# Performance work log

Hardware: AMD Instinct MI355X
Metric: run time of the kernel (lower is better)

## Reference

```python
import jax, jax.numpy as jnp
import numpy as np

N_GAUSS, H, W, SH_DEG = 1024, 256, 256, 3

SH_C0 = 0.28209479177387814
SH_C1 = 0.4886025119029199
SH_C2 = (1.0925484305920792, -1.0925484305920792, 0.31539156525252005,
         -1.0925484305920792, 0.5462742152960396)
SH_C3 = (-0.5900435899266435, 2.890611442640554, -0.4570457994644658,
         0.3731763325901154, -0.4570457994644658, 1.445305721320277,
         -0.5900435899266435)


def eval_sh(shs, dirs):
    # shs: [N,16,3], dirs: [N,3] normalized. Matches computeColorFromSH (deg 3).
    x, y, z = dirs[:, 0:1], dirs[:, 1:2], dirs[:, 2:3]
    res = SH_C0 * shs[:, 0]
    res = res - SH_C1 * y * shs[:, 1] + SH_C1 * z * shs[:, 2] - SH_C1 * x * shs[:, 3]
    xx, yy, zz = x * x, y * y, z * z
    xy, yz, xz = x * y, y * z, x * z
    res = (res + SH_C2[0] * xy * shs[:, 4] + SH_C2[1] * yz * shs[:, 5]
           + SH_C2[2] * (2.0 * zz - xx - yy) * shs[:, 6]
           + SH_C2[3] * xz * shs[:, 7] + SH_C2[4] * (xx - yy) * shs[:, 8])
    res = (res + SH_C3[0] * y * (3.0 * xx - yy) * shs[:, 9]
           + SH_C3[1] * xy * z * shs[:, 10]
           + SH_C3[2] * y * (4.0 * zz - xx - yy) * shs[:, 11]
           + SH_C3[3] * z * (2.0 * zz - 3.0 * xx - 3.0 * yy) * shs[:, 12]
           + SH_C3[4] * x * (4.0 * zz - xx - yy) * shs[:, 13]
           + SH_C3[5] * z * (xx - yy) * shs[:, 14]
           + SH_C3[6] * x * (xx - yy - zz) * shs[:, 15])
    return jnp.maximum(res + 0.5, 0.0)


def render(background, means3D, opacities, scales, rotations, shs,
           view_mat, proj_mat, cam_pos, tan_fovx, tan_fovy, height, width):
    N = means3D.shape[0]
    tanx, tany = tan_fovx[0], tan_fovy[0]
    fx = width / (2.0 * tanx)
    fy = height / (2.0 * tany)

    # --- 3D covariance: Sigma = R diag(s^2) R^T (computeCov3D) ---
    q = rotations / jnp.linalg.norm(rotations, axis=-1, keepdims=True)
    r, x, y, z = q[:, 0], q[:, 1], q[:, 2], q[:, 3]
    R = jnp.stack([
        jnp.stack([1 - 2 * (y * y + z * z), 2 * (x * y - r * z), 2 * (x * z + r * y)], -1),
        jnp.stack([2 * (x * y + r * z), 1 - 2 * (x * x + z * z), 2 * (y * z - r * x)], -1),
        jnp.stack([2 * (x * z - r * y), 2 * (y * z + r * x), 1 - 2 * (x * x + y * y)], -1),
    ], -2)  # [N,3,3]
    M = R * scales[:, None, :]
    Sigma = jnp.einsum('nij,nkj->nik', M, M)  # [N,3,3]

    # --- view transform + EWA 2D covariance (computeCov2D) ---
    t = means3D @ view_mat[:3, :3].T + view_mat[:3, 3]  # [N,3] camera space
    tz = t[:, 2]
    valid_z = tz > 0.2
    tzs = jnp.where(valid_z, tz, 1.0)
    limx, limy = 1.3 * tanx, 1.3 * tany
    tx = jnp.clip(t[:, 0] / tzs, -limx, limx) * tzs
    ty = jnp.clip(t[:, 1] / tzs, -limy, limy) * tzs
    zeros = jnp.zeros_like(tzs)
    J = jnp.stack([
        jnp.stack([fx / tzs, zeros, -fx * tx / (tzs * tzs)], -1),
        jnp.stack([zeros, fy / tzs, -fy * ty / (tzs * tzs)], -1),
    ], -2)  # [N,2,3]
    T2 = jnp.einsum('nij,jk->nik', J, view_mat[:3, :3])
    cov2d = jnp.einsum('nij,njk,nlk->nil', T2, Sigma, T2)  # [N,2,2]
    a = cov2d[:, 0, 0] + 0.3
    c = cov2d[:, 1, 1] + 0.3
    b = cov2d[:, 0, 1]
    det = a * c - b * b
    valid = valid_z & (det > 0)
    inv_det = jnp.where(det > 0, 1.0 / jnp.where(det > 0, det, 1.0), 0.0)
    conic = jnp.stack([c, -b, a], -1) * inv_det[:, None]  # [N,3]

    # --- projection to pixel coords (ndc2Pix) ---
    ph = jnp.concatenate([means3D, jnp.ones((N, 1), means3D.dtype)], -1) @ proj_mat.T
    p_w = 1.0 / (ph[:, 3] + 1e-7)
    px = ((ph[:, 0] * p_w + 1.0) * width - 1.0) * 0.5
    py = ((ph[:, 1] * p_w + 1.0) * height - 1.0) * 0.5

    # --- SH -> RGB ---
    dirs = means3D - cam_pos[None, :]
    dirs = dirs / jnp.linalg.norm(dirs, axis=-1, keepdims=True)
    colors = eval_sh(shs, dirs)  # [N,3]

    # --- global depth sort (front to back) ---
    depth = jnp.where(valid, tz, 1e10)
    order = jnp.argsort(depth)
    px_s, py_s = px[order], py[order]
    conic_s = conic[order]
    opac_s = opacities[order, 0]
    colors_s = colors[order]
    valid_s = valid[order]

    # --- per-pixel alpha and front-to-back compositing (renderCUDA) ---
    ys, xs = jnp.meshgrid(jnp.arange(height, dtype=jnp.float32),
                          jnp.arange(width, dtype=jnp.float32), indexing='ij')
    pixx, pixy = xs.reshape(-1), ys.reshape(-1)  # [P]
    dx = px_s[:, None] - pixx[None, :]  # [N,P]
    dy = py_s[:, None] - pixy[None, :]
    power = (-0.5 * (conic_s[:, 0:1] * dx * dx + conic_s[:, 2:3] * dy * dy)
             - conic_s[:, 1:2] * dx * dy)
    alpha = jnp.minimum(opac_s[:, None] * jnp.exp(jnp.minimum(power, 0.0)), 0.99)
    keep = (power <= 0.0) & (alpha >= 1.0 / 255.0) & valid_s[:, None]
    alpha = jnp.where(keep, alpha, 0.0)

    Tcum = jnp.cumprod(1.0 - alpha, axis=0)  # [N,P]
    T_prev = jnp.concatenate([jnp.ones((1, alpha.shape[1]), alpha.dtype), Tcum[:-1]], 0)
    wgt = alpha * T_prev
    img = jnp.einsum('nc,np->cp', colors_s, wgt) + background[:, None] * Tcum[-1][None, :]
    return img.reshape(3, height, width)


def setup_inputs() -> dict:
    key = jax.random.key(0)
    ks = jax.random.split(key, 6)
    means3D = jax.random.uniform(ks[0], (N_GAUSS, 3), minval=-3.0, maxval=3.0)
    means3D = means3D.at[:, 2].set(
        jax.random.uniform(ks[1], (N_GAUSS,), minval=2.0, maxval=10.0))
    opacities = jax.random.uniform(ks[2], (N_GAUSS, 1), minval=0.3, maxval=0.95)
    scales = jax.random.uniform(ks[3], (N_GAUSS, 3), minval=0.02, maxval=0.15)
    rotations = jax.random.normal(ks[4], (N_GAUSS, 4))
    shs = jax.random.normal(ks[5], (N_GAUSS, (SH_DEG + 1) ** 2, 3)) * 0.3
    background = jnp.zeros((3,), jnp.float32)
    view_mat = jnp.eye(4, dtype=jnp.float32)  # camera at origin looking +z
    tanx = tany = 0.5
    zn, zf = 0.01, 100.0
    proj = np.zeros((4, 4), np.float32)
    proj[0, 0] = 1.0 / tanx
    proj[1, 1] = 1.0 / tany
    proj[2, 2] = zf / (zf - zn)
    proj[2, 3] = -(zf * zn) / (zf - zn)
    proj[3, 2] = 1.0
    proj_mat = jnp.asarray(proj) @ view_mat  # full projection
    cam_pos = jnp.zeros((3,), jnp.float32)
    return dict(background=background, means3D=means3D, opacities=opacities,
                scales=scales, rotations=rotations, shs=shs, view_mat=view_mat,
                proj_mat=proj_mat, cam_pos=cam_pos,
                tan_fovx=jnp.array([tanx], jnp.float32),
                tan_fovy=jnp.array([tany], jnp.float32), height=H, width=W)


def reference(background, means3D, opacities, scales, rotations, shs,
              view_mat, proj_mat, cam_pos, tan_fovx, tan_fovy, height, width):
    return render(background, means3D, opacities, scales, rotations, shs,
                  view_mat, proj_mat, cam_pos, tan_fovx, tan_fovy, height, width)
```

## Files before the change

kernel.cpp:

```cpp
#include <hip/hip_runtime.h>
#include <math.h>

#define NG 1024
#define LOG2E 1.4426950408889634f


__global__ void prep_kernel(
    const float* __restrict__ means3D, const float* __restrict__ opacities,
    const float* __restrict__ scales,  const float* __restrict__ rotations,
    const float* __restrict__ shs,     const float* __restrict__ view_mat,
    const float* __restrict__ proj_mat,const float* __restrict__ cam_pos,
    const float* __restrict__ tanx_p,  const float* __restrict__ tany_p,
    const int* __restrict__ h_p,       const int* __restrict__ w_p,
    unsigned long long* __restrict__ grec, float4* __restrict__ rec, int N)
{
    int i = blockIdx.x * blockDim.x + threadIdx.x;
    if (i >= N) return;
    float tanx = tanx_p[0], tany = tany_p[0];
    float Wf = (float)w_p[0], Hf = (float)h_p[0];
    int tilesX = w_p[0] >> 3, tilesY = h_p[0] >> 3;
    float fx = Wf / (2.f * tanx), fy = Hf / (2.f * tany);

    float mx = means3D[3*i], my = means3D[3*i+1], mz = means3D[3*i+2];

    float4 q4 = ((const float4*)rotations)[i];
    float qr = q4.x, qx = q4.y, qy = q4.z, qz = q4.w;
    float qn = sqrtf(qr*qr + qx*qx + qy*qy + qz*qz);
    qr /= qn; qx /= qn; qy /= qn; qz /= qn;
    float sx = scales[3*i], sy = scales[3*i+1], sz = scales[3*i+2];
    float R00 = 1.f-2.f*(qy*qy+qz*qz), R01 = 2.f*(qx*qy-qr*qz), R02 = 2.f*(qx*qz+qr*qy);
    float R10 = 2.f*(qx*qy+qr*qz), R11 = 1.f-2.f*(qx*qx+qz*qz), R12 = 2.f*(qy*qz-qr*qx);
    float R20 = 2.f*(qx*qz-qr*qy), R21 = 2.f*(qy*qz+qr*qx), R22 = 1.f-2.f*(qx*qx+qy*qy);
    float M00=R00*sx, M01=R01*sy, M02=R02*sz;
    float M10=R10*sx, M11=R11*sy, M12=R12*sz;
    float M20=R20*sx, M21=R21*sy, M22=R22*sz;
    float S00 = M00*M00+M01*M01+M02*M02;
    float S01 = M00*M10+M01*M11+M02*M12;
    float S02 = M00*M20+M01*M21+M02*M22;
    float S11 = M10*M10+M11*M11+M12*M12;
    float S12 = M10*M20+M11*M21+M12*M22;
    float S22 = M20*M20+M21*M21+M22*M22;

    const float* V = view_mat;
    float t0 = V[0]*mx + V[1]*my + V[2]*mz  + V[3];
    float t1 = V[4]*mx + V[5]*my + V[6]*mz  + V[7];
    float t2 = V[8]*mx + V[9]*my + V[10]*mz + V[11];
    bool valid_z = t2 > 0.2f;
    float tzs = valid_z ? t2 : 1.0f;
    float limx = 1.3f*tanx, limy = 1.3f*tany;
    float txc = fminf(fmaxf(t0/tzs, -limx), limx) * tzs;
    float tyc = fminf(fmaxf(t1/tzs, -limy), limy) * tzs;
    float inv_tz = 1.f / tzs;
    float J00 = fx*inv_tz, J02 = -fx*txc*inv_tz*inv_tz;
    float J11 = fy*inv_tz, J12 = -fy*tyc*inv_tz*inv_tz;
    float T200 = J00*V[0] + J02*V[8];
    float T201 = J00*V[1] + J02*V[9];
    float T202 = J00*V[2] + J02*V[10];
    float T210 = J11*V[4] + J12*V[8];
    float T211 = J11*V[5] + J12*V[9];
    float T212 = J11*V[6] + J12*V[10];
    float u0 = S00*T200 + S01*T201 + S02*T202;
    float u1 = S01*T200 + S11*T201 + S12*T202;
    float u2 = S02*T200 + S12*T201 + S22*T202;
    float cov00 = T200*u0 + T201*u1 + T202*u2;
    float cov01 = T210*u0 + T211*u1 + T212*u2;
    float v0 = S00*T210 + S01*T211 + S02*T212;
    float v1 = S01*T210 + S11*T211 + S12*T212;
    float v2 = S02*T210 + S12*T211 + S22*T212;
    float cov11 = T210*v0 + T211*v1 + T212*v2;
    float a = cov00 + 0.3f;
    float c = cov11 + 0.3f;
    float b = cov01;
    float det = a*c - b*b;
    bool valid = valid_z && (det > 0.f);
    float inv_det = (det > 0.f) ? (1.f/det) : 0.f;
    float Aq = c*inv_det, Bq = -b*inv_det, Cq = a*inv_det;

    const float* P = proj_mat;
    float ph0 = P[0]*mx  + P[1]*my  + P[2]*mz  + P[3];
    float ph1 = P[4]*mx  + P[5]*my  + P[6]*mz  + P[7];
    float ph3 = P[12]*mx + P[13]*my + P[14]*mz + P[15];
    float pw = 1.f / (ph3 + 1e-7f);
    float px = ((ph0*pw + 1.f)*Wf - 1.f)*0.5f;
    float py = ((ph1*pw + 1.f)*Hf - 1.f)*0.5f;

    float dxm = mx - cam_pos[0], dym = my - cam_pos[1], dzm = mz - cam_pos[2];
    float dn = sqrtf(dxm*dxm + dym*dym + dzm*dzm);
    float X = dxm/dn, Y = dym/dn, Z = dzm/dn;
    float xx = X*X, yy = Y*Y, zz = Z*Z;
    float xy = X*Y, yz = Y*Z, xz = X*Z;
    float sc[48];
    {
        const float4* s4 = (const float4*)(shs + i*48);
        #pragma unroll
        for (int k = 0; k < 12; k++) {
            float4 v = s4[k];
            sc[4*k] = v.x; sc[4*k+1] = v.y; sc[4*k+2] = v.z; sc[4*k+3] = v.w;
        }
    }
    float col[3];
    #pragma unroll
    for (int ch = 0; ch < 3; ch++) {
        float res = 0.28209479177387814f * sc[ch];
        res += -0.4886025119029199f * Y * sc[3+ch]
             +  0.4886025119029199f * Z * sc[6+ch]
             -  0.4886025119029199f * X * sc[9+ch];
        res +=  1.0925484305920792f * xy * sc[12+ch]
             + (-1.0925484305920792f) * yz * sc[15+ch]
             +  0.31539156525252005f * (2.f*zz - xx - yy) * sc[18+ch]
             + (-1.0925484305920792f) * xz * sc[21+ch]
             +  0.5462742152960396f * (xx - yy) * sc[24+ch];
        res += -0.5900435899266435f * Y * (3.f*xx - yy) * sc[27+ch]
             +  2.890611442640554f  * xy * Z * sc[30+ch]
             + (-0.4570457994644658f) * Y * (4.f*zz - xx - yy) * sc[33+ch]
             +  0.3731763325901154f  * Z * (2.f*zz - 3.f*xx - 3.f*yy) * sc[36+ch]
             + (-0.4570457994644658f) * X * (4.f*zz - xx - yy) * sc[39+ch]
             +  1.445305721320277f   * Z * (xx - yy) * sc[42+ch]
             + (-0.5900435899266435f) * X * (xx - yy - zz) * sc[45+ch];
        col[ch] = fmaxf(res + 0.5f, 0.f);
    }

    float op = valid ? opacities[i] : 0.f;
    float dpt = valid ? t2 : 1e10f;

    float tau = 2.f * logf(255.f * fmaxf(op, 1e-20f));
    bool has = valid && (op * 255.f > 1.f) && (tau > 0.f);
    float rx = has ? (sqrtf(tau * a) + 0.01f) : 0.f;
    float ry = has ? (sqrtf(tau * c) + 0.01f) : 0.f;

    unsigned trange = 31u;
    if (has) {
        int tx0 = (int)ceilf((px - rx - 7.f) * 0.125f);
        int tx1 = (int)floorf((px + rx) * 0.125f);
        int ty0 = (int)ceilf((py - ry - 7.f) * 0.125f);
        int ty1 = (int)floorf((py + ry) * 0.125f);
        tx0 = max(tx0, 0); ty0 = max(ty0, 0);
        tx1 = min(tx1, tilesX - 1); ty1 = min(ty1, tilesY - 1);
        if (tx0 <= tx1 && ty0 <= ty1)
            trange = (unsigned)tx0 | ((unsigned)tx1 << 5)
                   | ((unsigned)ty0 << 10) | ((unsigned)ty1 << 15);
    }
    grec[i] = ((unsigned long long)__float_as_uint(dpt) << 32)
            | ((unsigned long long)(unsigned)i << 20) | trange;

    rec[i*3 + 0] = make_float4(px, py, -0.5f*LOG2E*Aq, -LOG2E*Bq);
    rec[i*3 + 1] = make_float4(-0.5f*LOG2E*Cq, op, col[0], col[1]);
    rec[i*3 + 2] = make_float4(col[2], 0.f, 0.f, 0.f);
}

__device__ inline unsigned long long bstage_shfl(unsigned long long key,
                                                 int tid, int j, int k) {
    unsigned long long partner = __shfl_xor(key, j, 64);
    bool lower = (tid & j) == 0;
    bool asc   = (tid & k) == 0;
    return ((key < partner) == (lower == asc)) ? key : partner;
}

__device__ inline float rlane(float v, int l) {
    return __int_as_float(__builtin_amdgcn_readlane(__float_as_int(v), l));
}

__global__ void __launch_bounds__(64) render_kernel(
    const unsigned long long* __restrict__ grec,
    const float4* __restrict__ rec,
    const float* __restrict__ background,
    float* __restrict__ out,
    int N, int W, int HW)
{
    __shared__ unsigned long long skey[NG];
    int tile = blockIdx.x;
    int tilesX = W >> 3;
    int tx = tile % tilesX, ty = tile / tilesX;
    int lane = threadIdx.x;
    int lx = lane & 7, ly = lane >> 3;
    float pixx = (float)(tx*8 + lx);
    float pixy = (float)(ty*8 + ly);

    int cnt = 0;
    const unsigned long long missk = 31ull;
    for (int base = 0; base < N; base += 256) {
        int g0 = base + lane;
        unsigned long long ka = (g0       < N) ? grec[g0]       : missk;
        unsigned long long kb = (g0 + 64  < N) ? grec[g0 + 64]  : missk;
        unsigned long long kc = (g0 + 128 < N) ? grec[g0 + 128] : missk;
        unsigned long long kd = (g0 + 192 < N) ? grec[g0 + 192] : missk;
        #pragma unroll
        for (int s = 0; s < 4; s++) {
            unsigned long long k = (s == 0) ? ka : (s == 1) ? kb : (s == 2) ? kc : kd;
            unsigned tr = (unsigned)k;
            bool hit = (tx >= (int)(tr & 31u)) & (tx <= (int)((tr >> 5) & 31u))
                     & (ty >= (int)((tr >> 10) & 31u)) & (ty <= (int)((tr >> 15) & 31u));
            unsigned long long mask = __ballot(hit);
            if (hit) {
                int pos = cnt + __popcll(mask & ((1ull << lane) - 1ull));
                skey[pos] = k;
            }
            cnt += __popcll(mask);
        }
    }
    __syncthreads();

    float T = 1.f, Cr = 0.f, Cg = 0.f, Cb = 0.f;
    if (cnt > 0 && cnt <= 64) {
        unsigned long long key = (lane < cnt) ? skey[lane] : ~0ull;
        for (int k = 2; k <= 64; k <<= 1)
            for (int j = k >> 1; j >= 1; j >>= 1)
                key = bstage_shfl(key, lane, j, k);
        int gg = (int)((key >> 20) & (NG - 1));
        float4 r0 = rec[gg*3 + 0];
        float4 r1 = rec[gg*3 + 1];
        float4 r2 = rec[gg*3 + 2];
        for (int m = 0; m < cnt; m++) {
            float gpx = rlane(r0.x, m), gpy = rlane(r0.y, m);
            float gA  = rlane(r0.z, m), gB  = rlane(r0.w, m);
            float gC  = rlane(r1.x, m), gop = rlane(r1.y, m);
            float gcr = rlane(r1.z, m), gcg = rlane(r1.w, m);
            float gcb = rlane(r2.x, m);
            float dx = gpx - pixx, dy = gpy - pixy;
            float p2 = fmaf(gA, dx*dx, fmaf(gC, dy*dy, gB*(dx*dy)));
            float e  = __builtin_amdgcn_exp2f(p2);
            float alpha = fminf(gop * e, 0.99f);
            float a2 = (alpha >= (1.f/255.f)) ? alpha : 0.f;
            float w = a2 * T;
            Cr = fmaf(gcr, w, Cr);
            Cg = fmaf(gcg, w, Cg);
            Cb = fmaf(gcb, w, Cb);
            T  = T - a2 * T;
            if ((m & 15) == 15 && __all(T < 1e-4f)) break;
        }
    } else if (cnt > 64) {
        int P = 128;
        while (P < cnt) P <<= 1;
        for (int i2 = cnt + lane; i2 < P; i2 += 64) skey[i2] = ~0ull;
        __syncthreads();
        for (int k = 2; k <= P; k <<= 1) {
            for (int j = k >> 1; j >= 1; j >>= 1) {
                for (int i2 = lane; i2 < P; i2 += 64) {
                    int ixj = i2 ^ j;
                    if (ixj > i2) {
                        bool asc = (i2 & k) == 0;
                        unsigned long long u = skey[i2], v = skey[ixj];
                        if ((u > v) == asc) { skey[i2] = v; skey[ixj] = u; }
                    }
                }
                __syncthreads();
            }
        }
        bool dead = false;
        for (int c = 0; c < cnt && !dead; c += 64) {
            int len = min(64, cnt - c);
            int idx = c + lane;
            int gg = 0;
            if (idx < cnt) gg = (int)((skey[idx] >> 20) & (NG - 1));
            float4 r0 = rec[gg*3 + 0];
            float4 r1 = rec[gg*3 + 1];
            float4 r2 = rec[gg*3 + 2];
            for (int m = 0; m < len; m++) {
                float gpx = rlane(r0.x, m), gpy = rlane(r0.y, m);
                float gA  = rlane(r0.z, m), gB  = rlane(r0.w, m);
                float gC  = rlane(r1.x, m), gop = rlane(r1.y, m);
                float gcr = rlane(r1.z, m), gcg = rlane(r1.w, m);
                float gcb = rlane(r2.x, m);
                float dx = gpx - pixx, dy = gpy - pixy;
                float p2 = fmaf(gA, dx*dx, fmaf(gC, dy*dy, gB*(dx*dy)));
                float e  = __builtin_amdgcn_exp2f(p2);
                float alpha = fminf(gop * e, 0.99f);
                float a2 = (alpha >= (1.f/255.f)) ? alpha : 0.f;
                float w = a2 * T;
                Cr = fmaf(gcr, w, Cr);
                Cg = fmaf(gcg, w, Cg);
                Cb = fmaf(gcb, w, Cb);
                T  = T - a2 * T;
                if ((m & 15) == 15 && __all(T < 1e-4f)) { dead = true; break; }
            }
            if (__all(T < 1e-4f)) dead = true;
        }
    }

    int p = (ty*8 + ly) * W + tx*8 + lx;
    out[p]        = Cr + background[0]*T;
    out[HW + p]   = Cg + background[1]*T;
    out[2*HW + p] = Cb + background[2]*T;
}

extern "C" void kernel_launch(void* const* d_in, const int* in_sizes, int n_in,
                              void* d_out, int out_size, void* d_ws, size_t ws_size,
                              hipStream_t stream) {
    const float* background = (const float*)d_in[0];
    const float* means3D    = (const float*)d_in[1];
    const float* opacities  = (const float*)d_in[2];
    const float* scales     = (const float*)d_in[3];
    const float* rotations  = (const float*)d_in[4];
    const float* shs        = (const float*)d_in[5];
    const float* view_mat   = (const float*)d_in[6];
    const float* proj_mat   = (const float*)d_in[7];
    const float* cam_pos    = (const float*)d_in[8];
    const float* tanx       = (const float*)d_in[9];
    const float* tany       = (const float*)d_in[10];
    const int*   hp         = (const int*)d_in[11];
    const int*   wp         = (const int*)d_in[12];

    int N  = in_sizes[2];
    int HW = out_size / 3;
    int W  = 256;
    int H  = HW / W;
    float* out = (float*)d_out;

    unsigned long long* grec = (unsigned long long*)d_ws;
    float4* rec = (float4*)(grec + NG);

    prep_kernel<<<16, 64, 0, stream>>>(
        means3D, opacities, scales, rotations, shs, view_mat, proj_mat,
        cam_pos, tanx, tany, hp, wp, grec, rec, N);

    int tiles = (W >> 3) * (H >> 3);
    render_kernel<<<tiles, 64, 0, stream>>>(
        grec, rec, background, out, N, W, HW);
}
```

Baseline: 18.35 us.

## Fuse preprocessing into render kernel, recomputing Gaussian geometry per tile

Removes the separate prep kernel and its global record buffers. Each 8x8 tile block recomputes projection and conic geometry for all 1024 Gaussians to cull them against its own bounds, then recomputes full attributes, including SH color, only for the Gaussians that hit. This trades one kernel launch and a global round trip for heavily redundant per-tile arithmetic (1024 tiles times 1024 Gaussians). The cull now tests a float bounding box rather than integer tile ranges, which can change borderline tile membership.

```diff
diff --git a/kernel.cpp b/kernel.cpp
--- a/kernel.cpp
+++ b/kernel.cpp
@@ -5,22 +5,30 @@
 #define LOG2E 1.4426950408889634f
 
 
-__global__ void prep_kernel(
+__device__ inline unsigned long long bstage_shfl(unsigned long long key,
+                                                 int tid, int j, int k) {
+    unsigned long long partner = __shfl_xor(key, j, 64);
+    bool lower = (tid & j) == 0;
+    bool asc   = (tid & k) == 0;
+    return ((key < partner) == (lower == asc)) ? key : partner;
+}
+
+__device__ inline float rlane(float v, int l) {
+    return __int_as_float(__builtin_amdgcn_readlane(__float_as_int(v), l));
+}
+
+struct Geo {
+    float px, py, rx, ry, dpt, a, b, c, op;
+    bool has;
+};
+
+__device__ inline Geo compute_geo(
+    int i,
     const float* __restrict__ means3D, const float* __restrict__ opacities,
     const float* __restrict__ scales,  const float* __restrict__ rotations,
-    const float* __restrict__ shs,     const float* __restrict__ view_mat,
-    const float* __restrict__ proj_mat,const float* __restrict__ cam_pos,
-    const float* __restrict__ tanx_p,  const float* __restrict__ tany_p,
-    const int* __restrict__ h_p,       const int* __restrict__ w_p,
-    unsigned long long* __restrict__ grec, float4* __restrict__ rec, int N)
+    const float* __restrict__ V,       const float* __restrict__ P,
+    float tanx, float tany, float fx, float fy, float Wf, float Hf)
 {
-    int i = blockIdx.x * blockDim.x + threadIdx.x;
-    if (i >= N) return;
-    float tanx = tanx_p[0], tany = tany_p[0];
-    float Wf = (float)w_p[0], Hf = (float)h_p[0];
-    int tilesX = w_p[0] >> 3, tilesY = h_p[0] >> 3;
-    float fx = Wf / (2.f * tanx), fy = Hf / (2.f * tany);
-
     float mx = means3D[3*i], my = means3D[3*i+1], mz = means3D[3*i+2];
 
     float4 q4 = ((const float4*)rotations)[i];
@@ -41,7 +49,6 @@
     float S12 = M10*M20+M11*M21+M12*M22;
     float S22 = M20*M20+M21*M21+M22*M22;
 
-    const float* V = view_mat;
     float t0 = V[0]*mx + V[1]*my + V[2]*mz  + V[3];
     float t1 = V[4]*mx + V[5]*my + V[6]*mz  + V[7];
     float t2 = V[8]*mx + V[9]*my + V[10]*mz + V[11];
@@ -68,22 +75,51 @@
     float v1 = S01*T210 + S11*T211 + S12*T212;
     float v2 = S02*T210 + S12*T211 + S22*T212;
     float cov11 = T210*v0 + T211*v1 + T212*v2;
-    float a = cov00 + 0.3f;
-    float c = cov11 + 0.3f;
-    float b = cov01;
-    float det = a*c - b*b;
+
+    Geo g;
+    g.a = cov00 + 0.3f;
+    g.c = cov11 + 0.3f;
+    g.b = cov01;
+    float det = g.a*g.c - g.b*g.b;
     bool valid = valid_z && (det > 0.f);
-    float inv_det = (det > 0.f) ? (1.f/det) : 0.f;
-    float Aq = c*inv_det, Bq = -b*inv_det, Cq = a*inv_det;
-
-    const float* P = proj_mat;
+
     float ph0 = P[0]*mx  + P[1]*my  + P[2]*mz  + P[3];
     float ph1 = P[4]*mx  + P[5]*my  + P[6]*mz  + P[7];
     float ph3 = P[12]*mx + P[13]*my + P[14]*mz + P[15];
     float pw = 1.f / (ph3 + 1e-7f);
-    float px = ((ph0*pw + 1.f)*Wf - 1.f)*0.5f;
-    float py = ((ph1*pw + 1.f)*Hf - 1.f)*0.5f;
-
+    g.px = ((ph0*pw + 1.f)*Wf - 1.f)*0.5f;
+    g.py = ((ph1*pw + 1.f)*Hf - 1.f)*0.5f;
+
+    g.op  = valid ? opacities[i] : 0.f;
+    g.dpt = valid ? t2 : 1e10f;
+
+    float tau = 2.f * logf(255.f * fmaxf(g.op, 1e-20f));
+    bool has = valid && (g.op * 255.f > 1.f) && (tau > 0.f);
+    g.rx = has ? (sqrtf(tau * g.a) + 0.01f) : 0.f;
+    g.ry = has ? (sqrtf(tau * g.c) + 0.01f) : 0.f;
+    g.has = has;
+    return g;
+}
+
+__device__ inline void compute_full(
+    int i,
+    const float* __restrict__ means3D, const float* __restrict__ opacities,
+    const float* __restrict__ scales,  const float* __restrict__ rotations,
+    const float* __restrict__ shs,     const float* __restrict__ cam_pos,
+    const float* __restrict__ V,       const float* __restrict__ P,
+    float tanx, float tany, float fx, float fy, float Wf, float Hf,
+    float& px, float& py, float& A2, float& B2, float& C2,
+    float& op, float& cr, float& cg, float& cb)
+{
+    Geo g = compute_geo(i, means3D, opacities, scales, rotations, V, P,
+                        tanx, tany, fx, fy, Wf, Hf);
+    float det = g.a*g.c - g.b*g.b;
+    float inv_det = (det > 0.f) ? (1.f/det) : 0.f;
+    float Aq = g.c*inv_det, Bq = -g.b*inv_det, Cq = g.a*inv_det;
+    px = g.px; py = g.py; op = g.op;
+    A2 = -0.5f*LOG2E*Aq; B2 = -LOG2E*Bq; C2 = -0.5f*LOG2E*Cq;
+
+    float mx = means3D[3*i], my = means3D[3*i+1], mz = means3D[3*i+2];
     float dxm = mx - cam_pos[0], dym = my - cam_pos[1], dzm = mz - cam_pos[2];
     float dn = sqrtf(dxm*dxm + dym*dym + dzm*dzm);
     float X = dxm/dn, Y = dym/dn, Z = dzm/dn;
@@ -119,52 +155,17 @@
              + (-0.5900435899266435f) * X * (xx - yy - zz) * sc[45+ch];
         col[ch] = fmaxf(res + 0.5f, 0.f);
     }
-
-    float op = valid ? opacities[i] : 0.f;
-    float dpt = valid ? t2 : 1e10f;
-
-    float tau = 2.f * logf(255.f * fmaxf(op, 1e-20f));
-    bool has = valid && (op * 255.f > 1.f) && (tau > 0.f);
-    float rx = has ? (sqrtf(tau * a) + 0.01f) : 0.f;
-    float ry = has ? (sqrtf(tau * c) + 0.01f) : 0.f;
-
-    unsigned trange = 31u;
-    if (has) {
-        int tx0 = (int)ceilf((px - rx - 7.f) * 0.125f);
-        int tx1 = (int)floorf((px + rx) * 0.125f);
-        int ty0 = (int)ceilf((py - ry - 7.f) * 0.125f);
-        int ty1 = (int)floorf((py + ry) * 0.125f);
-        tx0 = max(tx0, 0); ty0 = max(ty0, 0);
-        tx1 = min(tx1, tilesX - 1); ty1 = min(ty1, tilesY - 1);
-        if (tx0 <= tx1 && ty0 <= ty1)
-            trange = (unsigned)tx0 | ((unsigned)tx1 << 5)
-                   | ((unsigned)ty0 << 10) | ((unsigned)ty1 << 15);
-    }
-    grec[i] = ((unsigned long long)__float_as_uint(dpt) << 32)
-            | ((unsigned long long)(unsigned)i << 20) | trange;
-
-    rec[i*3 + 0] = make_float4(px, py, -0.5f*LOG2E*Aq, -LOG2E*Bq);
-    rec[i*3 + 1] = make_float4(-0.5f*LOG2E*Cq, op, col[0], col[1]);
-    rec[i*3 + 2] = make_float4(col[2], 0.f, 0.f, 0.f);
-}
-
-__device__ inline unsigned long long bstage_shfl(unsigned long long key,
-                                                 int tid, int j, int k) {
-    unsigned long long partner = __shfl_xor(key, j, 64);
-    bool lower = (tid & j) == 0;
-    bool asc   = (tid & k) == 0;
-    return ((key < partner) == (lower == asc)) ? key : partner;
-}
-
-__device__ inline float rlane(float v, int l) {
-    return __int_as_float(__builtin_amdgcn_readlane(__float_as_int(v), l));
-}
-
-__global__ void __launch_bounds__(64) render_kernel(
-    const unsigned long long* __restrict__ grec,
-    const float4* __restrict__ rec,
-    const float* __restrict__ background,
-    float* __restrict__ out,
+    cr = col[0]; cg = col[1]; cb = col[2];
+}
+
+__global__ void __launch_bounds__(64) fused_kernel(
+    const float* __restrict__ means3D, const float* __restrict__ opacities,
+    const float* __restrict__ scales,  const float* __restrict__ rotations,
+    const float* __restrict__ shs,     const float* __restrict__ view_mat,
+    const float* __restrict__ proj_mat,const float* __restrict__ cam_pos,
+    const float* __restrict__ tanx_p,  const float* __restrict__ tany_p,
+    const int* __restrict__ h_p,       const int* __restrict__ w_p,
+    const float* __restrict__ background, float* __restrict__ out,
     int N, int W, int HW)
 {
     __shared__ unsigned long long skey[NG];
@@ -175,28 +176,34 @@
     int lx = lane & 7, ly = lane >> 3;
     float pixx = (float)(tx*8 + lx);
     float pixy = (float)(ty*8 + ly);
+    float x0 = (float)(tx*8), x1 = x0 + 7.f;
+    float y0 = (float)(ty*8), y1 = y0 + 7.f;
+
+    float tanx = tanx_p[0], tany = tany_p[0];
+    float Wf = (float)w_p[0], Hf = (float)h_p[0];
+    float fx = Wf / (2.f * tanx), fy = Hf / (2.f * tany);
+    const float* V = view_mat;
+    const float* P = proj_mat;
 
     int cnt = 0;
-    const unsigned long long missk = 31ull;
-    for (int base = 0; base < N; base += 256) {
-        int g0 = base + lane;
-        unsigned long long ka = (g0       < N) ? grec[g0]       : missk;
-        unsigned long long kb = (g0 + 64  < N) ? grec[g0 + 64]  : missk;
-        unsigned long long kc = (g0 + 128 < N) ? grec[g0 + 128] : missk;
-        unsigned long long kd = (g0 + 192 < N) ? grec[g0 + 192] : missk;
-        #pragma unroll
-        for (int s = 0; s < 4; s++) {
-            unsigned long long k = (s == 0) ? ka : (s == 1) ? kb : (s == 2) ? kc : kd;
-            unsigned tr = (unsigned)k;
-            bool hit = (tx >= (int)(tr & 31u)) & (tx <= (int)((tr >> 5) & 31u))
-                     & (ty >= (int)((tr >> 10) & 31u)) & (ty <= (int)((tr >> 15) & 31u));
-            unsigned long long mask = __ballot(hit);
-            if (hit) {
-                int pos = cnt + __popcll(mask & ((1ull << lane) - 1ull));
-                skey[pos] = k;
-            }
-            cnt += __popcll(mask);
-        }
+    for (int base = 0; base < N; base += 64) {
+        int gi = base + lane;
+        bool hit = false;
+        float dpt = 0.f;
+        if (gi < N) {
+            Geo g = compute_geo(gi, means3D, opacities, scales, rotations,
+                                V, P, tanx, tany, fx, fy, Wf, Hf);
+            hit = g.has & (g.px - g.rx <= x1) & (g.px + g.rx >= x0)
+                        & (g.py - g.ry <= y1) & (g.py + g.ry >= y0);
+            dpt = g.dpt;
+        }
+        unsigned long long mask = __ballot(hit);
+        if (hit) {
+            int pos = cnt + __popcll(mask & ((1ull << lane) - 1ull));
+            skey[pos] = ((unsigned long long)__float_as_uint(dpt) << 32)
+                      | (unsigned)gi;
+        }
+        cnt += __popcll(mask);
     }
     __syncthreads();
 
@@ -206,16 +213,17 @@
         for (int k = 2; k <= 64; k <<= 1)
             for (int j = k >> 1; j >= 1; j >>= 1)
                 key = bstage_shfl(key, lane, j, k);
-        int gg = (int)((key >> 20) & (NG - 1));
-        float4 r0 = rec[gg*3 + 0];
-        float4 r1 = rec[gg*3 + 1];
-        float4 r2 = rec[gg*3 + 2];
+        int gg = (int)((unsigned)key & (NG - 1));
+        float gpx_, gpy_, gA_, gB_, gC_, gop_, gcr_, gcg_, gcb_;
+        compute_full(gg, means3D, opacities, scales, rotations, shs, cam_pos,
+                     V, P, tanx, tany, fx, fy, Wf, Hf,
+                     gpx_, gpy_, gA_, gB_, gC_, gop_, gcr_, gcg_, gcb_);
         for (int m = 0; m < cnt; m++) {
-            float gpx = rlane(r0.x, m), gpy = rlane(r0.y, m);
-            float gA  = rlane(r0.z, m), gB  = rlane(r0.w, m);
-            float gC  = rlane(r1.x, m), gop = rlane(r1.y, m);
-            float gcr = rlane(r1.z, m), gcg = rlane(r1.w, m);
-            float gcb = rlane(r2.x, m);
+            float gpx = rlane(gpx_, m), gpy = rlane(gpy_, m);
+            float gA  = rlane(gA_, m),  gB  = rlane(gB_, m);
+            float gC  = rlane(gC_, m),  gop = rlane(gop_, m);
+            float gcr = rlane(gcr_, m), gcg = rlane(gcg_, m);
+            float gcb = rlane(gcb_, m);
             float dx = gpx - pixx, dy = gpy - pixy;
             float p2 = fmaf(gA, dx*dx, fmaf(gC, dy*dy, gB*(dx*dy)));
             float e  = __builtin_amdgcn_exp2f(p2);
@@ -229,13 +237,13 @@
             if ((m & 15) == 15 && __all(T < 1e-4f)) break;
         }
     } else if (cnt > 64) {
-        int P = 128;
-        while (P < cnt) P <<= 1;
-        for (int i2 = cnt + lane; i2 < P; i2 += 64) skey[i2] = ~0ull;
+        int Pp = 128;
+        while (Pp < cnt) Pp <<= 1;
+        for (int i2 = cnt + lane; i2 < Pp; i2 += 64) skey[i2] = ~0ull;
         __syncthreads();
-        for (int k = 2; k <= P; k <<= 1) {
+        for (int k = 2; k <= Pp; k <<= 1) {
             for (int j = k >> 1; j >= 1; j >>= 1) {
-                for (int i2 = lane; i2 < P; i2 += 64) {
+                for (int i2 = lane; i2 < Pp; i2 += 64) {
                     int ixj = i2 ^ j;
                     if (ixj > i2) {
                         bool asc = (i2 & k) == 0;
@@ -251,16 +259,17 @@
             int len = min(64, cnt - c);
             int idx = c + lane;
             int gg = 0;
-            if (idx < cnt) gg = (int)((skey[idx] >> 20) & (NG - 1));
-            float4 r0 = rec[gg*3 + 0];
-            float4 r1 = rec[gg*3 + 1];
-            float4 r2 = rec[gg*3 + 2];
+            if (idx < cnt) gg = (int)((unsigned)skey[idx] & (NG - 1));
+            float gpx_, gpy_, gA_, gB_, gC_, gop_, gcr_, gcg_, gcb_;
+            compute_full(gg, means3D, opacities, scales, rotations, shs, cam_pos,
+                         V, P, tanx, tany, fx, fy, Wf, Hf,
+                         gpx_, gpy_, gA_, gB_, gC_, gop_, gcr_, gcg_, gcb_);
             for (int m = 0; m < len; m++) {
-                float gpx = rlane(r0.x, m), gpy = rlane(r0.y, m);
-                float gA  = rlane(r0.z, m), gB  = rlane(r0.w, m);
-                float gC  = rlane(r1.x, m), gop = rlane(r1.y, m);
-                float gcr = rlane(r1.z, m), gcg = rlane(r1.w, m);
-                float gcb = rlane(r2.x, m);
+                float gpx = rlane(gpx_, m), gpy = rlane(gpy_, m);
+                float gA  = rlane(gA_, m),  gB  = rlane(gB_, m);
+                float gC  = rlane(gC_, m),  gop = rlane(gop_, m);
+                float gcr = rlane(gcr_, m), gcg = rlane(gcg_, m);
+                float gcb = rlane(gcb_, m);
                 float dx = gpx - pixx, dy = gpy - pixy;
                 float p2 = fmaf(gA, dx*dx, fmaf(gC, dy*dy, gB*(dx*dy)));
                 float e  = __builtin_amdgcn_exp2f(p2);
@@ -306,14 +315,8 @@
     int H  = HW / W;
     float* out = (float*)d_out;
 
-    unsigned long long* grec = (unsigned long long*)d_ws;
-    float4* rec = (float4*)(grec + NG);
-
-    prep_kernel<<<16, 64, 0, stream>>>(
+    int tiles = (W >> 3) * (H >> 3);
+    fused_kernel<<<tiles, 64, 0, stream>>>(
         means3D, opacities, scales, rotations, shs, view_mat, proj_mat,
-        cam_pos, tanx, tany, hp, wp, grec, rec, N);
-
-    int tiles = (W >> 3) * (H >> 3);
-    render_kernel<<<tiles, 64, 0, stream>>>(
-        grec, rec, background, out, N, W, HW);
-}
+        cam_pos, tanx, tany, hp, wp, background, out, N, W, HW);
+}
```

After: 28.17 us. 1.54x slower.
